# Kernel optimization log

Measured on AMD Instinct MI355X. Metric: run time of the kernel, lower is better.

Reference implementation:

```python
import jax, jax.numpy as jnp
import numpy as np

N_TOKENS = 2048
D_IN = 1024
D_HID = 4096
D_OUT = 1024
N_EXPERTS = 8
TOP_K = 2


def setup_inputs() -> dict:
    key = jax.random.key(0)
    ks = jax.random.split(key, 8)
    s_in = 1.0 / np.sqrt(D_IN)
    s_hid = 1.0 / np.sqrt(D_HID)
    return {
        "x": jax.random.normal(ks[0], (N_TOKENS, D_IN), dtype=jnp.float32),
        # Router Linear(D_IN, E)
        "Wr": jax.random.uniform(ks[1], (D_IN, N_EXPERTS), jnp.float32, -s_in, s_in),
        "br": jax.random.uniform(ks[2], (N_EXPERTS,), jnp.float32, -s_in, s_in),
        # Stacked expert MLP weights [E, ...]
        "W1": jax.random.uniform(ks[3], (N_EXPERTS, D_IN, D_HID), jnp.float32, -s_in, s_in),
        "b1": jax.random.uniform(ks[4], (N_EXPERTS, D_HID), jnp.float32, -s_in, s_in),
        "W2": jax.random.uniform(ks[5], (N_EXPERTS, D_HID, D_OUT), jnp.float32, -s_hid, s_hid),
        "b2": jax.random.uniform(ks[6], (N_EXPERTS, D_OUT), jnp.float32, -s_hid, s_hid),
    }


def reference(x, Wr, br, W1, b1, W2, b2):
    # Router: softmax over expert logits, then top-k
    routing = jax.nn.softmax(x @ Wr + br, axis=-1)            # [N, E]
    topk_w, topk_idx = jax.lax.top_k(routing, TOP_K)          # [N, k] each
    # Combine weights per expert: c[n, e] = sum_i topk_w[n, i] * (topk_idx[n, i] == e)
    onehot = jax.nn.one_hot(topk_idx, N_EXPERTS, dtype=x.dtype)  # [N, k, E]
    combine = jnp.einsum('nk,nke->ne', topk_w, onehot)           # [N, E]
    # Run all experts on all tokens (dense equivalent of the dispatch loop);
    # non-selected experts get combine weight 0, so math matches exactly.
    h = jax.nn.relu(jnp.einsum('nd,edh->neh', x, W1) + b1)       # [N, E, H]
    y = jnp.einsum('neh,ehd->ned', h, W2) + b2                   # [N, E, Dout]
    out = jnp.einsum('ne,ned->nd', combine, y)                   # [N, Dout]
    return out
```

## Files before the change

kernel.cpp:

```cpp
#include <hip/hip_runtime.h>
#include <hip/hip_bf16.h>

#define N_TOKENS 2048
#define D_IN 1024
#define D_HID 4096
#define D_OUT 1024
#define NE 8

typedef __attribute__((ext_vector_type(8))) short s16x8;
typedef __attribute__((ext_vector_type(4))) float f32x4;

__device__ inline unsigned short f2bf(float f) {
  union { float f; unsigned u; } v; v.f = f;
  unsigned u = v.u;
  unsigned r = u + 0x7fff + ((u >> 16) & 1);
  return (unsigned short)(r >> 16);
}

#define GLDS16(gp, lp)                                                          \
  __builtin_amdgcn_global_load_lds(                                             \
      (const __attribute__((address_space(1))) unsigned int*)(gp),              \
      (__attribute__((address_space(3))) unsigned int*)(lp), 16, 0, 0)

__global__ __launch_bounds__(256) void router_kernel(
    const float* __restrict__ x, const float* __restrict__ Wr,
    const float* __restrict__ br, int* __restrict__ cnt, int* __restrict__ tids,
    int4* __restrict__ meta, float2* __restrict__ tw) {
  int wid = threadIdx.x >> 6, lane = threadIdx.x & 63;
  int n = blockIdx.x * 4 + wid;
  const float* xr = x + (size_t)n * D_IN;
  float acc[NE];
#pragma unroll
  for (int e = 0; e < NE; e++) acc[e] = 0.f;
  for (int i = lane; i < D_IN; i += 64) {
    float xv = xr[i];
    const float4* wr = (const float4*)(Wr + (size_t)i * NE);
    float4 w0 = wr[0], w1 = wr[1];
    acc[0] += xv * w0.x; acc[1] += xv * w0.y;
    acc[2] += xv * w0.z; acc[3] += xv * w0.w;
    acc[4] += xv * w1.x; acc[5] += xv * w1.y;
    acc[6] += xv * w1.z; acc[7] += xv * w1.w;
  }
#pragma unroll
  for (int e = 0; e < NE; e++) {
#pragma unroll
    for (int s = 32; s; s >>= 1) acc[e] += __shfl_xor(acc[e], s, 64);
  }
  if (lane == 0) {
    float lg[NE], p[NE];
    float m = -1e30f;
#pragma unroll
    for (int e = 0; e < NE; e++) { lg[e] = acc[e] + br[e]; m = fmaxf(m, lg[e]); }
    float s = 0.f;
#pragma unroll
    for (int e = 0; e < NE; e++) { p[e] = expf(lg[e] - m); s += p[e]; }
    float inv = 1.f / s;
    int i0 = 0;
#pragma unroll
    for (int e = 1; e < NE; e++) if (lg[e] > lg[i0]) i0 = e;
    int i1 = (i0 == 0) ? 1 : 0;
#pragma unroll
    for (int e = 0; e < NE; e++) if (e != i0 && lg[e] > lg[i1]) i1 = e;
    int p0 = atomicAdd(&cnt[i0], 1);
    int p1 = atomicAdd(&cnt[i1], 1);
    tids[i0 * N_TOKENS + p0] = n;
    tids[i1 * N_TOKENS + p1] = n;
    meta[n] = make_int4(i0, p0, i1, p1);
    tw[n] = make_float2(p[i0] * inv, p[i1] * inv);
  }
}

__global__ __launch_bounds__(256) void convx_kernel(const float* __restrict__ x,
                                                    short* __restrict__ xb) {
  int i = (blockIdx.x * 256 + threadIdx.x) * 4;
  float4 v = *(const float4*)(x + i);
  short4 o;
  o.x = (short)f2bf(v.x); o.y = (short)f2bf(v.y);
  o.z = (short)f2bf(v.z); o.w = (short)f2bf(v.w);
  *(short4*)(xb + i) = o;
}

__global__ __launch_bounds__(256) void transconv_kernel(
    const float* __restrict__ src, short* __restrict__ dst, int R, int C) {
  __shared__ float tile[64][65];
  int tx = threadIdx.x & 63, ty = threadIdx.x >> 6;
  size_t eoff = (size_t)blockIdx.z * R * C;
  int r0 = blockIdx.y * 64, c0 = blockIdx.x * 64;
  const float* s = src + eoff + (size_t)r0 * C + c0;
#pragma unroll
  for (int i = 0; i < 16; i++) {
    int r = i * 4 + ty;
    tile[r][tx] = s[(size_t)r * C + tx];
  }
  __syncthreads();
  short* d = dst + eoff + (size_t)c0 * R + r0;
#pragma unroll
  for (int i = 0; i < 16; i++) {
    int c = i * 4 + ty;
    d[(size_t)c * R + tx] = (short)f2bf(tile[tx][c]);
  }
}

__global__ __launch_bounds__(256) void gemm1_kernel(
    const short* __restrict__ xb,
    const short* __restrict__ W1b,
    const float* __restrict__ b1,
    const int* __restrict__ cnt, const int* __restrict__ tids,
    short* __restrict__ H) {
  const int NT_M = N_TOKENS / 128, NT_N = D_HID / 128;
  int bid0 = blockIdx.x;
  int bid = (bid0 & 7) * ((NE * NT_M * NT_N) >> 3) + (bid0 >> 3);
  int e = bid / (NT_M * NT_N);
  int r2 = bid % (NT_M * NT_N);
  int mt = r2 % NT_M, nt = r2 / NT_M;
  int ce = cnt[e];
  if (mt * 128 >= ce) return;
  int off = 0;
  for (int i = 0; i < e; i++) off += cnt[i];

  __shared__ alignas(16) short As[2][128][64];
  __shared__ alignas(16) short Bs[2][128][64];

  int lane = threadIdx.x & 63, wid = threadIdx.x >> 6;
  int wr = wid >> 1, wc = wid & 1;
  int lrow = lane >> 3;
  int ach = ((lane & 7) ^ lrow) * 8;

  const int* tlist = tids + e * N_TOKENS + mt * 128;
  const short* agp[4];
  const short* bgp[4];
#pragma unroll
  for (int c = 0; c < 4; c++) {
    int r = c * 32 + wid * 8 + lrow;
    int t = (mt * 128 + r < ce) ? tlist[r] : tlist[0];
    agp[c] = xb + (size_t)t * D_IN + ach;
    bgp[c] = W1b + (size_t)e * D_HID * D_IN + (size_t)(nt * 128 + r) * D_IN + ach;
  }

  f32x4 zero = {0.f, 0.f, 0.f, 0.f};
  f32x4 acc[4][4];
#pragma unroll
  for (int i = 0; i < 4; i++) {
#pragma unroll
    for (int j = 0; j < 4; j++) acc[i][j] = zero;
  }

#define STAGE1(ks, buf)                                                         \
  {                                                                             \
    int k0 = (ks) * 64;                                                         \
    _Pragma("unroll")                                                           \
    for (int c = 0; c < 4; c++) {                                               \
      GLDS16(agp[c] + k0, &As[buf][c * 32 + wid * 8][0]);                       \
      GLDS16(bgp[c] + k0, &Bs[buf][c * 32 + wid * 8][0]);                       \
    }                                                                           \
  }

  const int NK = D_IN / 64;
  STAGE1(0, 0);
  __syncthreads();
  int cur = 0;
  for (int ks = 0; ks < NK; ks++) {
    if (ks + 1 < NK) STAGE1(ks + 1, cur ^ 1);
#pragma unroll
    for (int kk = 0; kk < 2; kk++) {
      s16x8 a[4], b[4];
      int ch = ((kk * 4 + (lane >> 4)) ^ (lane & 7)) * 8;
#pragma unroll
      for (int i = 0; i < 4; i++)
        a[i] = *(const s16x8*)&As[cur][wr * 64 + i * 16 + (lane & 15)][ch];
#pragma unroll
      for (int j = 0; j < 4; j++)
        b[j] = *(const s16x8*)&Bs[cur][wc * 64 + j * 16 + (lane & 15)][ch];
#pragma unroll
      for (int i = 0; i < 4; i++) {
#pragma unroll
        for (int j = 0; j < 4; j++)
          acc[i][j] = __builtin_amdgcn_mfma_f32_16x16x32_bf16(a[i], b[j], acc[i][j], 0, 0, 0);
      }
    }
    __syncthreads();
    cur ^= 1;
  }

  int lr = (lane >> 4) * 4, lc = lane & 15;
#pragma unroll
  for (int j = 0; j < 4; j++) {
    int col = nt * 128 + wc * 64 + j * 16 + lc;
    float bias = b1[e * D_HID + col];
#pragma unroll
    for (int i = 0; i < 4; i++) {
#pragma unroll
      for (int r = 0; r < 4; r++) {
        int grow = mt * 128 + wr * 64 + i * 16 + lr + r;
        if (grow < ce) {
          float v = fmaxf(acc[i][j][r] + bias, 0.f);
          H[(size_t)(off + grow) * D_HID + col] = (short)f2bf(v);
        }
      }
    }
  }
}

__global__ __launch_bounds__(256) void gemm2_kernel(
    const short* __restrict__ H,
    const short* __restrict__ W2b,
    const int* __restrict__ cnt,
    float* __restrict__ Y) {
  const int NT_M = N_TOKENS / 128, NT_N = D_OUT / 128;
  int bid0 = blockIdx.x;
  int bid = (bid0 & 7) * ((NE * NT_M * NT_N) >> 3) + (bid0 >> 3);
  int e = bid / (NT_M * NT_N);
  int r2 = bid % (NT_M * NT_N);
  int mt = r2 % NT_M, nt = r2 / NT_M;
  int ce = cnt[e];
  if (mt * 128 >= ce) return;
  int off = 0;
  for (int i = 0; i < e; i++) off += cnt[i];

  __shared__ alignas(16) short As[2][128][64];
  __shared__ alignas(16) short Bs[2][128][64];

  int lane = threadIdx.x & 63, wid = threadIdx.x >> 6;
  int wr = wid >> 1, wc = wid & 1;
  int lrow = lane >> 3;
  int ach = ((lane & 7) ^ lrow) * 8;

  const short* agp[4];
  const short* bgp[4];
#pragma unroll
  for (int c = 0; c < 4; c++) {
    int r = c * 32 + wid * 8 + lrow;
    int grow = mt * 128 + r;
    if (grow > ce - 1) grow = ce - 1;
    agp[c] = H + (size_t)(off + grow) * D_HID + ach;
    bgp[c] = W2b + (size_t)e * D_OUT * D_HID + (size_t)(nt * 128 + r) * D_HID + ach;
  }

  f32x4 zero = {0.f, 0.f, 0.f, 0.f};
  f32x4 acc[4][4];
#pragma unroll
  for (int i = 0; i < 4; i++) {
#pragma unroll
    for (int j = 0; j < 4; j++) acc[i][j] = zero;
  }

#define STAGE2(ks, buf)                                                         \
  {                                                                             \
    int k0 = (ks) * 64;                                                         \
    _Pragma("unroll")                                                           \
    for (int c = 0; c < 4; c++) {                                               \
      GLDS16(agp[c] + k0, &As[buf][c * 32 + wid * 8][0]);                       \
      GLDS16(bgp[c] + k0, &Bs[buf][c * 32 + wid * 8][0]);                       \
    }                                                                           \
  }

  const int NK = D_HID / 64;
  STAGE2(0, 0);
  __syncthreads();
  int cur = 0;
  for (int ks = 0; ks < NK; ks++) {
    if (ks + 1 < NK) STAGE2(ks + 1, cur ^ 1);
#pragma unroll
    for (int kk = 0; kk < 2; kk++) {
      s16x8 a[4], b[4];
      int ch = ((kk * 4 + (lane >> 4)) ^ (lane & 7)) * 8;
#pragma unroll
      for (int i = 0; i < 4; i++)
        a[i] = *(const s16x8*)&As[cur][wr * 64 + i * 16 + (lane & 15)][ch];
#pragma unroll
      for (int j = 0; j < 4; j++)
        b[j] = *(const s16x8*)&Bs[cur][wc * 64 + j * 16 + (lane & 15)][ch];
#pragma unroll
      for (int i = 0; i < 4; i++) {
#pragma unroll
        for (int j = 0; j < 4; j++)
          acc[i][j] = __builtin_amdgcn_mfma_f32_16x16x32_bf16(a[i], b[j], acc[i][j], 0, 0, 0);
      }
    }
    __syncthreads();
    cur ^= 1;
  }

  int lr = (lane >> 4) * 4, lc = lane & 15;
#pragma unroll
  for (int j = 0; j < 4; j++) {
    int col = nt * 128 + wc * 64 + j * 16 + lc;
#pragma unroll
    for (int i = 0; i < 4; i++) {
#pragma unroll
      for (int r = 0; r < 4; r++) {
        int grow = mt * 128 + wr * 64 + i * 16 + lr + r;
        if (grow < ce) Y[(size_t)(off + grow) * D_OUT + col] = acc[i][j][r];
      }
    }
  }
}

__global__ __launch_bounds__(256) void combine_kernel(
    const float* __restrict__ Y, const float* __restrict__ b2,
    const int* __restrict__ cnt, const int4* __restrict__ meta,
    const float2* __restrict__ tw, float* __restrict__ out) {
  int n = blockIdx.x;
  int4 m = meta[n];
  float2 w = tw[n];
  int off0 = 0, off1 = 0;
#pragma unroll
  for (int i = 0; i < NE; i++) {
    int c = cnt[i];
    if (i < m.x) off0 += c;
    if (i < m.z) off1 += c;
  }
  const float4* y0 = (const float4*)(Y + (size_t)(off0 + m.y) * D_OUT);
  const float4* y1 = (const float4*)(Y + (size_t)(off1 + m.w) * D_OUT);
  const float4* g0 = (const float4*)(b2 + (size_t)m.x * D_OUT);
  const float4* g1 = (const float4*)(b2 + (size_t)m.z * D_OUT);
  float4* o = (float4*)(out + (size_t)n * D_OUT);
  int d = threadIdx.x;
  float4 a = y0[d], b = y1[d], ba = g0[d], bb = g1[d];
  float4 r;
  r.x = w.x * (a.x + ba.x) + w.y * (b.x + bb.x);
  r.y = w.x * (a.y + ba.y) + w.y * (b.y + bb.y);
  r.z = w.x * (a.z + ba.z) + w.y * (b.z + bb.z);
  r.w = w.x * (a.w + ba.w) + w.y * (b.w + bb.w);
  o[d] = r;
}

extern "C" void kernel_launch(void* const* d_in, const int* in_sizes, int n_in,
                              void* d_out, int out_size, void* d_ws, size_t ws_size,
                              hipStream_t stream) {
  const float* x  = (const float*)d_in[0];
  const float* Wr = (const float*)d_in[1];
  const float* br = (const float*)d_in[2];
  const float* W1 = (const float*)d_in[3];
  const float* b1 = (const float*)d_in[4];
  const float* W2 = (const float*)d_in[5];
  const float* b2 = (const float*)d_in[6];
  float* out = (float*)d_out;

  char* ws = (char*)d_ws;
  size_t o = 0;
  auto alloc = [&](size_t bytes) -> void* {
    o = (o + 255) & ~(size_t)255;
    void* p = ws + o;
    o += bytes;
    return p;
  };
  int*    cnt  = (int*)alloc(NE * 4);
  int*    tids = (int*)alloc((size_t)NE * N_TOKENS * 4);
  int4*   meta = (int4*)alloc((size_t)N_TOKENS * 16);
  float2* tw   = (float2*)alloc((size_t)N_TOKENS * 8);
  short*  xb   = (short*)alloc((size_t)N_TOKENS * D_IN * 2);
  short*  W1b  = (short*)alloc((size_t)NE * D_HID * D_IN * 2);
  short*  W2b  = (short*)alloc((size_t)NE * D_OUT * D_HID * 2);
  short*  H    = (short*)alloc((size_t)2 * N_TOKENS * D_HID * 2);
  float*  Y    = (float*)alloc((size_t)2 * N_TOKENS * D_OUT * 4);
  if (o > ws_size) return;

  hipMemsetAsync(cnt, 0, NE * 4, stream);
  router_kernel<<<N_TOKENS / 4, 256, 0, stream>>>(x, Wr, br, cnt, tids, meta, tw);
  convx_kernel<<<(N_TOKENS * D_IN / 4) / 256, 256, 0, stream>>>(x, xb);
  transconv_kernel<<<dim3(D_HID / 64, D_IN / 64, NE), 256, 0, stream>>>(W1, W1b, D_IN, D_HID);
  transconv_kernel<<<dim3(D_OUT / 64, D_HID / 64, NE), 256, 0, stream>>>(W2, W2b, D_HID, D_OUT);
  gemm1_kernel<<<NE * (N_TOKENS / 128) * (D_HID / 128), 256, 0, stream>>>(xb, W1b, b1, cnt, tids, H);
  gemm2_kernel<<<NE * (N_TOKENS / 128) * (D_OUT / 128), 256, 0, stream>>>(H, W2b, cnt, Y);
  combine_kernel<<<N_TOKENS, 256, 0, stream>>>(Y, b2, cnt, meta, tw, out);
}
```

Measured before the change: 600.7 us.

## Deepen GEMM load pipeline with explicit vmcnt waits and vectorize transpose-convert

Both expert GEMM kernels now prefetch two K-stages ahead, issuing the next global-to-LDS load after the compute barrier. They replace __syncthreads with s_waitcnt vmcnt(8) plus a raw s_barrier, so a block waits only for the current stage's loads rather than draining all of them. The weight transpose-convert kernel now uses float4 loads and short4 stores instead of scalar accesses. The aim is to hide more global-load latency and cut memory-instruction count, but the hand-counted vmcnt depends on exactly 8 loads per stage, and the column reads from the 65-wide LDS tile may hit bank conflicts.

```diff
diff --git a/kernel.cpp b/kernel.cpp
--- a/kernel.cpp
+++ b/kernel.cpp
@@ -83,21 +83,32 @@
 __global__ __launch_bounds__(256) void transconv_kernel(
     const float* __restrict__ src, short* __restrict__ dst, int R, int C) {
   __shared__ float tile[64][65];
-  int tx = threadIdx.x & 63, ty = threadIdx.x >> 6;
   size_t eoff = (size_t)blockIdx.z * R * C;
   int r0 = blockIdx.y * 64, c0 = blockIdx.x * 64;
   const float* s = src + eoff + (size_t)r0 * C + c0;
-#pragma unroll
-  for (int i = 0; i < 16; i++) {
-    int r = i * 4 + ty;
-    tile[r][tx] = s[(size_t)r * C + tx];
+  int t = threadIdx.x;
+  int lc4 = (t & 15) * 4;
+  int lr16 = t >> 4;
+#pragma unroll
+  for (int p = 0; p < 4; p++) {
+    int r = p * 16 + lr16;
+    float4 v = *(const float4*)(s + (size_t)r * C + lc4);
+    tile[r][lc4 + 0] = v.x; tile[r][lc4 + 1] = v.y;
+    tile[r][lc4 + 2] = v.z; tile[r][lc4 + 3] = v.w;
   }
   __syncthreads();
   short* d = dst + eoff + (size_t)c0 * R + r0;
-#pragma unroll
-  for (int i = 0; i < 16; i++) {
-    int c = i * 4 + ty;
-    d[(size_t)c * R + tx] = (short)f2bf(tile[tx][c]);
+  int rr4 = (t & 15) * 4;
+  int cc = t >> 4;
+#pragma unroll
+  for (int p = 0; p < 4; p++) {
+    int c = p * 16 + cc;
+    short4 o;
+    o.x = (short)f2bf(tile[rr4 + 0][c]);
+    o.y = (short)f2bf(tile[rr4 + 1][c]);
+    o.z = (short)f2bf(tile[rr4 + 2][c]);
+    o.w = (short)f2bf(tile[rr4 + 3][c]);
+    *(short4*)(d + (size_t)c * R + rr4) = o;
   }
 }
 
@@ -157,10 +168,12 @@
 
   const int NK = D_IN / 64;
   STAGE1(0, 0);
-  __syncthreads();
+  STAGE1(1, 1);
   int cur = 0;
   for (int ks = 0; ks < NK; ks++) {
-    if (ks + 1 < NK) STAGE1(ks + 1, cur ^ 1);
+    if (ks + 1 < NK) asm volatile("s_waitcnt vmcnt(8)" : : : "memory");
+    else             asm volatile("s_waitcnt vmcnt(0)" : : : "memory");
+    __builtin_amdgcn_s_barrier();
 #pragma unroll
     for (int kk = 0; kk < 2; kk++) {
       s16x8 a[4], b[4];
@@ -178,7 +191,8 @@
           acc[i][j] = __builtin_amdgcn_mfma_f32_16x16x32_bf16(a[i], b[j], acc[i][j], 0, 0, 0);
       }
     }
-    __syncthreads();
+    __builtin_amdgcn_s_barrier();
+    if (ks + 2 < NK) STAGE1(ks + 2, cur);
     cur ^= 1;
   }
 
@@ -256,10 +270,12 @@
 
   const int NK = D_HID / 64;
   STAGE2(0, 0);
-  __syncthreads();
+  STAGE2(1, 1);
   int cur = 0;
   for (int ks = 0; ks < NK; ks++) {
-    if (ks + 1 < NK) STAGE2(ks + 1, cur ^ 1);
+    if (ks + 1 < NK) asm volatile("s_waitcnt vmcnt(8)" : : : "memory");
+    else             asm volatile("s_waitcnt vmcnt(0)" : : : "memory");
+    __builtin_amdgcn_s_barrier();
 #pragma unroll
     for (int kk = 0; kk < 2; kk++) {
       s16x8 a[4], b[4];
@@ -277,7 +293,8 @@
           acc[i][j] = __builtin_amdgcn_mfma_f32_16x16x32_bf16(a[i], b[j], acc[i][j], 0, 0, 0);
       }
     }
-    __syncthreads();
+    __builtin_amdgcn_s_barrier();
+    if (ks + 2 < NK) STAGE2(ks + 2, cur);
     cur ^= 1;
   }
 
```

Measured after the change: 579.2 us. 3.6% less time.
